# Kernel tuning notes

Hardware: AMD Instinct MI355X
Metric: run time of the kernel (lower is better)

The kernel has to match this reference:

```python
import jax, jax.numpy as jnp
import numpy as np

N_NODES, N_EDGES, HIDDEN, N_GRAPHS = 100000, 500000, 128, 2048
ATOM_DIM, BOND_DIM, OUT_DIM = 4, 3, 1


def setup_inputs() -> dict:
    key = jax.random.key(0)
    ks = jax.random.split(key, 13)
    s = 0.05  # small init scale to keep relu+scatter depth iterations numerically tame
    return {
        "x": jax.random.normal(ks[0], (N_NODES, ATOM_DIM), jnp.float32),
        "edge_index": jax.random.randint(ks[1], (2, N_EDGES), 0, N_NODES, dtype=jnp.int32),
        "edge_attr": jax.random.normal(ks[2], (N_EDGES, BOND_DIM), jnp.float32),
        "batch": jnp.sort(jax.random.randint(ks[3], (N_NODES,), 0, N_GRAPHS, dtype=jnp.int32)),
        "depth": 3,
        # DMPNN weights (bias=False)
        "W_i": jax.random.normal(ks[4], (HIDDEN, ATOM_DIM + BOND_DIM), jnp.float32) * s,
        "W_m": jax.random.normal(ks[5], (HIDDEN, HIDDEN), jnp.float32) * s,
        "W_a": jax.random.normal(ks[6], (HIDDEN, ATOM_DIM + HIDDEN), jnp.float32) * s,
        # FFN: Linear(d,4d) -> relu -> dropout(eval=identity) -> Linear(4d,d)
        "W1": jax.random.normal(ks[7], (4 * HIDDEN, HIDDEN), jnp.float32) * s,
        "b1": jnp.zeros((4 * HIDDEN,), jnp.float32),
        "W2": jax.random.normal(ks[8], (HIDDEN, 4 * HIDDEN), jnp.float32) * s,
        "b2": jnp.zeros((HIDDEN,), jnp.float32),
        "W_last": jax.random.normal(ks[9], (OUT_DIM, HIDDEN), jnp.float32) * s,
        "b_last": jnp.zeros((OUT_DIM,), jnp.float32),
    }


def reference(x, edge_index, edge_attr, batch, depth, W_i, W_m, W_a, W1, b1, W2, b2, W_last, b_last):
    src, dst = edge_index[0], edge_index[1]
    E = edge_attr.shape[0]
    N = x.shape[0]
    # h: per-edge state [E, H]
    h = jax.nn.relu(jnp.concatenate([x[src], edge_attr], axis=1) @ W_i.T)
    for _ in range(depth):
        # message: relu(W_m h) gathered at src, scatter-add to dst; PyG infers
        # dim_size from h (edge-level here), so aggregation buffer has E rows.
        m = jax.nn.relu(h @ W_m.T)
        h = h + jax.ops.segment_sum(m[src], dst, num_segments=E)
    # index_add_ edge states to nodes
    node_emb = jax.ops.segment_sum(h, dst, num_segments=N)  # [N, H]
    node_emb = jax.nn.relu(jnp.concatenate([x, node_emb], axis=1) @ W_a.T)
    # global_add_pool over graphs
    g = jax.ops.segment_sum(node_emb, batch, num_segments=N_GRAPHS)  # [G, H]
    g = jax.nn.relu(g @ W1.T + b1) @ W2.T + b2  # FFN (dropout eval = identity)
    return g @ W_last.T + b_last  # [G, OUT_DIM]
```

## Files before the change

kernel.cpp:

```cpp
#include <hip/hip_runtime.h>


#define NN 100000
#define NE 500000
#define HID 128
#define NG 2048
#define NB_SCAN 391

typedef __attribute__((ext_vector_type(8))) short bf16x8;
typedef __attribute__((ext_vector_type(4))) float f32x4;

__device__ __forceinline__ float b2f(ushort u) {
  return __uint_as_float(((uint)u) << 16);
}
__device__ __forceinline__ ushort f2b(float f) {
  uint u = __float_as_uint(f);
  return (ushort)((u + 0x7FFF + ((u >> 16) & 1)) >> 16);
}
__device__ __forceinline__ void acc8(float* a, bf16x8 v) {
#pragma unroll
  for (int j = 0; j < 8; ++j) a[j] += b2f((ushort)v[j]);
}
__device__ __forceinline__ bf16x8 pack8(const float* a) {
  bf16x8 o;
#pragma unroll
  for (int j = 0; j < 8; ++j) o[j] = (short)f2b(a[j]);
  return o;
}

__global__ __launch_bounds__(256) void k_convw(const float* __restrict__ Wm,
    const float* __restrict__ Wa, ushort* __restrict__ wmb, ushort* __restrict__ wab) {
  int i = blockIdx.x * 256 + threadIdx.x;
  if (i >= HID * HID) return;
  wmb[i] = f2b(Wm[i]);
  int c = i >> 7, k = i & 127;
  wab[i] = f2b(Wa[c * 132 + 4 + k]);
}

__global__ __launch_bounds__(256) void k_init_h(const int* __restrict__ src,
    const float* __restrict__ x, const float* __restrict__ ea,
    const float* __restrict__ Wi, ushort* __restrict__ h) {
  __shared__ float wis[HID * 7];
  for (int i = threadIdx.x; i < HID * 7; i += 256) wis[i] = Wi[i];
  __syncthreads();
  int idx = blockIdx.x * 256 + threadIdx.x;
  int e = idx >> 7, c = idx & 127;
  if (e >= NN) return;
  int s = src[e];
  const float* w = &wis[c * 7];
  float acc = x[s*4+0]*w[0] + x[s*4+1]*w[1] + x[s*4+2]*w[2] + x[s*4+3]*w[3]
            + ea[e*3+0]*w[4] + ea[e*3+1]*w[5] + ea[e*3+2]*w[6];
  h[(size_t)e * HID + c] = f2b(fmaxf(acc, 0.f));
}

__global__ __launch_bounds__(256) void k_hist2(const int* __restrict__ dst,
    int* __restrict__ cnt, int* __restrict__ cnt_lo) {
  int e = blockIdx.x * 256 + threadIdx.x;
  if (e >= NE) return;
  int d = dst[e];
  atomicAdd(&cnt[d], 1);
  if (e < NN) atomicAdd(&cnt_lo[d], 1);
}

__global__ __launch_bounds__(256) void k_scan1(const int* __restrict__ cnt,
    int* __restrict__ outp, int* __restrict__ bsums) {
  __shared__ int s[256];
  int t = threadIdx.x;
  int i = blockIdx.x * 256 + t;
  int v = (i < NN) ? cnt[i] : 0;
  s[t] = v;
  __syncthreads();
  for (int off = 1; off < 256; off <<= 1) {
    int u = (t >= off) ? s[t - off] : 0;
    __syncthreads();
    s[t] += u;
    __syncthreads();
  }
  if (i < NN) outp[i] = s[t] - v;
  if (t == 255) bsums[blockIdx.x] = s[255];
}

__global__ __launch_bounds__(512) void k_scan2(int* __restrict__ bsums) {
  __shared__ int s[512];
  int t = threadIdx.x;
  int v = (t < NB_SCAN) ? bsums[t] : 0;
  s[t] = v;
  __syncthreads();
  for (int off = 1; off < 512; off <<= 1) {
    int u = (t >= off) ? s[t - off] : 0;
    __syncthreads();
    s[t] += u;
    __syncthreads();
  }
  if (t < NB_SCAN) bsums[t] = s[t] - v;
}

__global__ __launch_bounds__(256) void k_scan3(int* __restrict__ outp,
                                               const int* __restrict__ bsums) {
  int i = blockIdx.x * 256 + threadIdx.x;
  if (i < NN) outp[i] += bsums[blockIdx.x];
  if (i == 0) outp[NN] = NE;
}

__global__ __launch_bounds__(256) void k_mid(const int* __restrict__ rowptr,
    const int* __restrict__ cnt_lo, int* __restrict__ midp) {
  int i = blockIdx.x * 256 + threadIdx.x;
  if (i < NN) midp[i] = rowptr[i] + cnt_lo[i];
}

__global__ __launch_bounds__(256) void k_fill2(const int* __restrict__ src,
    const int* __restrict__ dst, const int* __restrict__ rowptr,
    const int* __restrict__ midp, int* __restrict__ cur_lo,
    int* __restrict__ cur_hi, int* __restrict__ csr_src, int* __restrict__ csr_eid) {
  int e = blockIdx.x * 256 + threadIdx.x;
  if (e >= NE) return;
  int d = dst[e];
  int o;
  if (e < NN) o = rowptr[d] + atomicAdd(&cur_lo[d], 1);
  else        o = midp[d]   + atomicAdd(&cur_hi[d], 1);
  csr_src[o] = src[e];
  csr_eid[o] = e;
}

__global__ __launch_bounds__(256) void k_goff(const int* __restrict__ batch,
                                              int* __restrict__ goff) {
  int g = blockIdx.x * 256 + threadIdx.x;
  if (g > NG) return;
  int lo = 0, hi = NN;
  while (lo < hi) { int mid = (lo + hi) >> 1; if (batch[mid] < g) lo = mid + 1; else hi = mid; }
  goff[g] = lo;
}

template <bool HASX>
__global__ __launch_bounds__(256) void k_mfma(const ushort* __restrict__ A,
    const ushort* __restrict__ Wb, const float* __restrict__ X,
    const float* __restrict__ WaF, ushort* __restrict__ O, int nrows) {
  int tid = threadIdx.x;
  int wave = tid >> 6;
  int lane = tid & 63;
  int l15 = lane & 15, l4 = lane >> 4;
  int row0 = blockIdx.x * 64 + wave * 16;

  f32x4 acc[8];
#pragma unroll
  for (int ni = 0; ni < 8; ++ni) acc[ni] = (f32x4){0.f, 0.f, 0.f, 0.f};

  if (HASX) {
    float4 wv[8];
#pragma unroll
    for (int ni = 0; ni < 8; ++ni)
      wv[ni] = *reinterpret_cast<const float4*>(&WaF[(size_t)(ni * 16 + l15) * 132]);
#pragma unroll
    for (int j = 0; j < 4; ++j) {
      int r = row0 + l4 * 4 + j;
      if (r < nrows) {
        float4 xv = *reinterpret_cast<const float4*>(&X[(size_t)r * 4]);
#pragma unroll
        for (int ni = 0; ni < 8; ++ni)
          acc[ni][j] = xv.x * wv[ni].x + xv.y * wv[ni].y
                     + xv.z * wv[ni].z + xv.w * wv[ni].w;
      }
    }
  }

  const bf16x8 zero8 = {0, 0, 0, 0, 0, 0, 0, 0};
  int ar = row0 + l15;
#pragma unroll
  for (int k0 = 0; k0 < HID; k0 += 32) {
    bf16x8 a = (ar < nrows)
             ? *reinterpret_cast<const bf16x8*>(&A[(size_t)ar * HID + k0 + l4 * 8])
             : zero8;
    bf16x8 b[8];
#pragma unroll
    for (int ni = 0; ni < 8; ++ni)
      b[ni] = *reinterpret_cast<const bf16x8*>(&Wb[(size_t)(ni * 16 + l15) * HID + k0 + l4 * 8]);
#pragma unroll
    for (int ni = 0; ni < 8; ++ni)
      acc[ni] = __builtin_amdgcn_mfma_f32_16x16x32_bf16(a, b[ni], acc[ni], 0, 0, 0);
  }

#pragma unroll
  for (int j = 0; j < 4; ++j) {
    int r = row0 + l4 * 4 + j;
    if (r >= nrows) continue;
#pragma unroll
    for (int ni = 0; ni < 8; ++ni)
      O[(size_t)r * HID + ni * 16 + l15] = f2b(fmaxf(acc[ni][j], 0.f));
  }
}

__global__ __launch_bounds__(256) void k_gather8(const ushort* __restrict__ m,
    const int* __restrict__ rowptr, const int* __restrict__ csr_src,
    ushort* __restrict__ h) {
  int idx = blockIdx.x * 256 + threadIdx.x;
  int n = idx >> 4;
  if (n >= NN) return;
  int c8 = (idx & 15) * 8;
  float a[8];
  bf16x8 hv = *reinterpret_cast<const bf16x8*>(&h[(size_t)n * HID + c8]);
#pragma unroll
  for (int j = 0; j < 8; ++j) a[j] = b2f((ushort)hv[j]);
  int beg = rowptr[n], end = rowptr[n + 1];
  for (int i = beg; i < end; i += 8) {
    int ss[8];
#pragma unroll
    for (int k = 0; k < 8; ++k) ss[k] = csr_src[min(i + k, end - 1)];
    bf16x8 v[8];
#pragma unroll
    for (int k = 0; k < 8; ++k)
      v[k] = *reinterpret_cast<const bf16x8*>(&m[(size_t)ss[k] * HID + c8]);
#pragma unroll
    for (int k = 0; k < 8; ++k)
      if (i + k < end) acc8(a, v[k]);
  }
  *reinterpret_cast<bf16x8*>(&h[(size_t)n * HID + c8]) = pack8(a);
}

__device__ __forceinline__ void h0acc(float* a, const float w[8][7],
                                      float4 xv, float e0, float e1, float e2) {
#pragma unroll
  for (int j = 0; j < 8; ++j) {
    float t = xv.x*w[j][0] + xv.y*w[j][1] + xv.z*w[j][2] + xv.w*w[j][3]
            + e0*w[j][4] + e1*w[j][5] + e2*w[j][6];
    a[j] += fmaxf(t, 0.f);
  }
}

__global__ __launch_bounds__(256) void k_node_agg2(const ushort* __restrict__ h,
    const int* __restrict__ rowptr, const int* __restrict__ midp,
    const int* __restrict__ csr_src, const int* __restrict__ csr_eid,
    const float* __restrict__ x, const float* __restrict__ ea,
    const float* __restrict__ Wi, ushort* __restrict__ ne) {
  int idx = blockIdx.x * 256 + threadIdx.x;
  int n = idx >> 4;
  int c8 = (idx & 15) * 8;
  float w[8][7];
#pragma unroll
  for (int j = 0; j < 8; ++j)
#pragma unroll
    for (int k = 0; k < 7; ++k) w[j][k] = Wi[(c8 + j) * 7 + k];
  if (n >= NN) return;
  int beg = rowptr[n], mid = midp[n], end = rowptr[n + 1];
  float a[8];
#pragma unroll
  for (int j = 0; j < 8; ++j) a[j] = 0.f;

  for (int i = beg; i < mid; i += 4) {
    int ee[4];
#pragma unroll
    for (int k = 0; k < 4; ++k) ee[k] = csr_eid[min(i + k, mid - 1)];
    bf16x8 v[4];
#pragma unroll
    for (int k = 0; k < 4; ++k)
      v[k] = *reinterpret_cast<const bf16x8*>(&h[(size_t)ee[k] * HID + c8]);
#pragma unroll
    for (int k = 0; k < 4; ++k)
      if (i + k < mid) acc8(a, v[k]);
  }

  for (int i = mid; i < end; i += 4) {
    int s4[4], e4[4];
#pragma unroll
    for (int k = 0; k < 4; ++k) {
      int ii = min(i + k, end - 1);
      s4[k] = csr_src[ii];
      e4[k] = csr_eid[ii];
    }
    float4 xv[4];
    float ev[4][3];
#pragma unroll
    for (int k = 0; k < 4; ++k) {
      xv[k] = *reinterpret_cast<const float4*>(&x[(size_t)s4[k] * 4]);
      ev[k][0] = ea[(size_t)e4[k]*3+0];
      ev[k][1] = ea[(size_t)e4[k]*3+1];
      ev[k][2] = ea[(size_t)e4[k]*3+2];
    }
#pragma unroll
    for (int k = 0; k < 4; ++k)
      if (i + k < end) h0acc(a, w, xv[k], ev[k][0], ev[k][1], ev[k][2]);
  }
  *reinterpret_cast<bf16x8*>(&ne[(size_t)n * HID + c8]) = pack8(a);
}

__global__ __launch_bounds__(256) void k_pool(const ushort* __restrict__ na,
    const int* __restrict__ goff, float* __restrict__ g) {
  int idx = blockIdx.x * 256 + threadIdx.x;
  int gid = idx >> 4;
  if (gid >= NG) return;
  int c8 = (idx & 15) * 8;
  int beg = goff[gid], end = goff[gid + 1];
  float a[8];
#pragma unroll
  for (int j = 0; j < 8; ++j) a[j] = 0.f;
  for (int n = beg; n < end; ++n)
    acc8(a, *reinterpret_cast<const bf16x8*>(&na[(size_t)n * HID + c8]));
  *reinterpret_cast<float4*>(&g[(size_t)gid * HID + c8]) = make_float4(a[0], a[1], a[2], a[3]);
  *reinterpret_cast<float4*>(&g[(size_t)gid * HID + c8 + 4]) = make_float4(a[4], a[5], a[6], a[7]);
}

template <bool RELU>
__global__ __launch_bounds__(256) void k_gemm64(const float* __restrict__ A,
    const float* __restrict__ W, const float* __restrict__ bias,
    float* __restrict__ O, int nrows, int K, int N) {
  __shared__ float As[64][33];
  __shared__ float Bs[32][68];
  int tid = threadIdx.x;
  int row0 = blockIdx.x * 64;
  int col0 = blockIdx.y * 64;
  int tn = tid & 15;
  int tm = tid >> 4;
  float acc[4][4];
#pragma unroll
  for (int i = 0; i < 4; ++i)
#pragma unroll
    for (int j = 0; j < 4; ++j) acc[i][j] = 0.f;

  for (int k0 = 0; k0 < K; k0 += 32) {
    int ar = tid >> 3;
    int ak = (tid & 7) << 2;
#pragma unroll
    for (int rr = 0; rr < 2; ++rr) {
      int r = row0 + ar + rr * 32;
      float4 v = make_float4(0.f, 0.f, 0.f, 0.f);
      if (r < nrows) v = *reinterpret_cast<const float4*>(&A[(size_t)r * K + k0 + ak]);
      As[ar + rr*32][ak+0] = v.x; As[ar + rr*32][ak+1] = v.y;
      As[ar + rr*32][ak+2] = v.z; As[ar + rr*32][ak+3] = v.w;
    }
    int c = tid & 63;
    int kq = tid >> 6;
#pragma unroll
    for (int it = 0; it < 2; ++it) {
      int kk = kq * 4 + it * 16;
      float4 v = *reinterpret_cast<const float4*>(&W[(size_t)(col0 + c) * K + k0 + kk]);
      Bs[kk+0][c] = v.x; Bs[kk+1][c] = v.y; Bs[kk+2][c] = v.z; Bs[kk+3][c] = v.w;
    }
    __syncthreads();
#pragma unroll 8
    for (int k = 0; k < 32; ++k) {
      float av[4];
#pragma unroll
      for (int i = 0; i < 4; ++i) av[i] = As[tm*4 + i][k];
      float4 bv = *reinterpret_cast<const float4*>(&Bs[k][tn*4]);
#pragma unroll
      for (int i = 0; i < 4; ++i) {
        acc[i][0] = fmaf(av[i], bv.x, acc[i][0]);
        acc[i][1] = fmaf(av[i], bv.y, acc[i][1]);
        acc[i][2] = fmaf(av[i], bv.z, acc[i][2]);
        acc[i][3] = fmaf(av[i], bv.w, acc[i][3]);
      }
    }
    __syncthreads();
  }
#pragma unroll
  for (int i = 0; i < 4; ++i) {
    int r = row0 + tm * 4 + i;
    if (r >= nrows) continue;
    float4 o;
    int c = col0 + tn * 4;
    o.x = acc[i][0] + bias[c+0];
    o.y = acc[i][1] + bias[c+1];
    o.z = acc[i][2] + bias[c+2];
    o.w = acc[i][3] + bias[c+3];
    if (RELU) {
      o.x = fmaxf(o.x, 0.f); o.y = fmaxf(o.y, 0.f);
      o.z = fmaxf(o.z, 0.f); o.w = fmaxf(o.w, 0.f);
    }
    *reinterpret_cast<float4*>(&O[(size_t)r * N + c]) = o;
  }
}

__global__ __launch_bounds__(256) void k_last(const float* __restrict__ g3,
    const float* __restrict__ Wl, const float* __restrict__ bl,
    float* __restrict__ out) {
  int wid = (blockIdx.x * 256 + threadIdx.x) >> 6;
  int lane = threadIdx.x & 63;
  if (wid >= NG) return;
  float a = g3[(size_t)wid*128 + lane] * Wl[lane]
          + g3[(size_t)wid*128 + 64 + lane] * Wl[64 + lane];
  for (int off = 32; off; off >>= 1) a += __shfl_down(a, off);
  if (lane == 0) out[wid] = a + bl[0];
}

extern "C" void kernel_launch(void* const* d_in, const int* in_sizes, int n_in,
                              void* d_out, int out_size, void* d_ws, size_t ws_size,
                              hipStream_t stream) {
  const float* x    = (const float*)d_in[0];
  const int*   eidx = (const int*)d_in[1];
  const float* ea   = (const float*)d_in[2];
  const int*   batch= (const int*)d_in[3];
  const float* Wi   = (const float*)d_in[5];
  const float* Wm   = (const float*)d_in[6];
  const float* Wa   = (const float*)d_in[7];
  const float* W1   = (const float*)d_in[8];
  const float* b1   = (const float*)d_in[9];
  const float* W2   = (const float*)d_in[10];
  const float* b2   = (const float*)d_in[11];
  const float* Wl   = (const float*)d_in[12];
  const float* bl   = (const float*)d_in[13];
  float* out = (float*)d_out;

  const int* src = eidx;
  const int* dst = eidx + NE;

  char* p = (char*)d_ws;
  ushort* hb  = (ushort*)p; p += (size_t)NN * HID * 2;
  ushort* mb  = (ushort*)p; p += (size_t)NN * HID * 2;
  ushort* wmb = (ushort*)p; p += (size_t)HID * HID * 2;
  ushort* wab = (ushort*)p; p += (size_t)HID * HID * 2;
  float* g  = (float*)p; p += (size_t)NG * 128 * 4;
  float* g2 = (float*)p; p += (size_t)NG * 512 * 4;
  float* g3 = (float*)p; p += (size_t)NG * 128 * 4;
  int* csr_src = (int*)p; p += (size_t)NE * 4;
  int* csr_eid = (int*)p; p += (size_t)NE * 4;
  int* cnt    = (int*)p; p += (size_t)NN * 4;
  int* cnt_lo = (int*)p; p += (size_t)NN * 4;
  int* cur_lo = (int*)p; p += (size_t)NN * 4;
  int* cur_hi = (int*)p; p += (size_t)NN * 4;
  int* rowptr = (int*)p; p += (size_t)(NN + 4) * 4;
  int* midp   = (int*)p; p += (size_t)NN * 4;
  int* bsums  = (int*)p; p += 512 * 4;
  int* goff   = (int*)p; p += (size_t)(NG + 4) * 4;

  hipMemsetAsync(cnt, 0, (size_t)4 * NN * sizeof(int), stream);
  k_hist2<<<(NE + 255) / 256, 256, 0, stream>>>(dst, cnt, cnt_lo);
  k_scan1<<<NB_SCAN, 256, 0, stream>>>(cnt, rowptr, bsums);
  k_scan2<<<1, 512, 0, stream>>>(bsums);
  k_scan3<<<NB_SCAN, 256, 0, stream>>>(rowptr, bsums);
  k_mid  <<<NB_SCAN, 256, 0, stream>>>(rowptr, cnt_lo, midp);
  k_fill2<<<(NE + 255) / 256, 256, 0, stream>>>(src, dst, rowptr, midp,
                                                cur_lo, cur_hi, csr_src, csr_eid);
  k_goff <<<(NG + 256) / 256, 256, 0, stream>>>(batch, goff);

  k_convw<<<(HID * HID + 255) / 256, 256, 0, stream>>>(Wm, Wa, wmb, wab);

  k_init_h<<<(NN * HID) / 256, 256, 0, stream>>>(src, x, ea, Wi, hb);

  int ggrid = (NN + 63) / 64;
  int sgrid = (NN * 16 + 255) / 256;
  for (int it = 0; it < 3; ++it) {
    k_mfma<false><<<ggrid, 256, 0, stream>>>(hb, wmb, nullptr, nullptr, mb, NN);
    k_gather8<<<sgrid, 256, 0, stream>>>(mb, rowptr, csr_src, hb);
  }

  k_node_agg2<<<sgrid, 256, 0, stream>>>(hb, rowptr, midp, csr_src, csr_eid,
                                         x, ea, Wi, mb);
  k_mfma<true><<<ggrid, 256, 0, stream>>>(mb, wab, x, Wa, hb, NN);

  k_pool<<<(NG * 16 + 255) / 256, 256, 0, stream>>>(hb, goff, g);

  dim3 grid1((NG + 63) / 64, 512 / 64);
  k_gemm64<true><<<grid1, 256, 0, stream>>>(g, W1, b1, g2, NG, 128, 512);
  dim3 grid2((NG + 63) / 64, 128 / 64);
  k_gemm64<false><<<grid2, 256, 0, stream>>>(g2, W2, b2, g3, NG, 512, 128);
  k_last<<<(NG * 64) / 256, 256, 0, stream>>>(g3, Wl, bl, out);
}
```

Before: 485.3 us.

## Store edge/node features in 16-column planar layout for cache-local gathers

Measured after the change: 494.1 us. Within noise of the previous version (+1.8%).

```diff
diff --git a/kernel.cpp b/kernel.cpp
--- a/kernel.cpp
+++ b/kernel.cpp
@@ -6,6 +6,7 @@
 #define HID 128
 #define NG 2048
 #define NB_SCAN 391
+#define NBLKG 782
 
 typedef __attribute__((ext_vector_type(8))) short bf16x8;
 typedef __attribute__((ext_vector_type(4))) float f32x4;
@@ -26,6 +27,9 @@
 #pragma unroll
   for (int j = 0; j < 8; ++j) o[j] = (short)f2b(a[j]);
   return o;
+}
+__device__ __forceinline__ size_t taddr(int n, int c8) {
+  return ((size_t)(c8 >> 4) * NN + n) * 16 + (c8 & 8);
 }
 
 __global__ __launch_bounds__(256) void k_convw(const float* __restrict__ Wm,
@@ -39,7 +43,7 @@
 
 __global__ __launch_bounds__(256) void k_init_h(const int* __restrict__ src,
     const float* __restrict__ x, const float* __restrict__ ea,
-    const float* __restrict__ Wi, ushort* __restrict__ h) {
+    const float* __restrict__ Wi, ushort* __restrict__ hT) {
   __shared__ float wis[HID * 7];
   for (int i = threadIdx.x; i < HID * 7; i += 256) wis[i] = Wi[i];
   __syncthreads();
@@ -50,7 +54,7 @@
   const float* w = &wis[c * 7];
   float acc = x[s*4+0]*w[0] + x[s*4+1]*w[1] + x[s*4+2]*w[2] + x[s*4+3]*w[3]
             + ea[e*3+0]*w[4] + ea[e*3+1]*w[5] + ea[e*3+2]*w[6];
-  h[(size_t)e * HID + c] = f2b(fmaxf(acc, 0.f));
+  hT[((size_t)(c >> 4) * NN + e) * 16 + (c & 15)] = f2b(fmaxf(acc, 0.f));
 }
 
 __global__ __launch_bounds__(256) void k_hist2(const int* __restrict__ dst,
@@ -138,66 +142,88 @@
   int tid = threadIdx.x;
   int wave = tid >> 6;
   int lane = tid & 63;
+  int wr = wave >> 1, wc = wave & 1;
+  int row0 = blockIdx.x * 64 + wr * 32;
+  int col0 = wc * 64;
   int l15 = lane & 15, l4 = lane >> 4;
-  int row0 = blockIdx.x * 64 + wave * 16;
-
-  f32x4 acc[8];
-#pragma unroll
-  for (int ni = 0; ni < 8; ++ni) acc[ni] = (f32x4){0.f, 0.f, 0.f, 0.f};
+
+  f32x4 acc[2][4];
+#pragma unroll
+  for (int mi = 0; mi < 2; ++mi)
+#pragma unroll
+    for (int ni = 0; ni < 4; ++ni) acc[mi][ni] = (f32x4){0.f, 0.f, 0.f, 0.f};
 
   if (HASX) {
-    float4 wv[8];
-#pragma unroll
-    for (int ni = 0; ni < 8; ++ni)
-      wv[ni] = *reinterpret_cast<const float4*>(&WaF[(size_t)(ni * 16 + l15) * 132]);
+    float4 wv[4];
+#pragma unroll
+    for (int ni = 0; ni < 4; ++ni)
+      wv[ni] = *reinterpret_cast<const float4*>(&WaF[(size_t)(col0 + ni * 16 + l15) * 132]);
+#pragma unroll
+    for (int mi = 0; mi < 2; ++mi)
+#pragma unroll
+      for (int j = 0; j < 4; ++j) {
+        int r = row0 + mi * 16 + l4 * 4 + j;
+        if (r < nrows) {
+          float4 xv = *reinterpret_cast<const float4*>(&X[(size_t)r * 4]);
+#pragma unroll
+          for (int ni = 0; ni < 4; ++ni)
+            acc[mi][ni][j] = xv.x * wv[ni].x + xv.y * wv[ni].y
+                           + xv.z * wv[ni].z + xv.w * wv[ni].w;
+        }
+      }
+  }
+
+  const bf16x8 zero8 = {0, 0, 0, 0, 0, 0, 0, 0};
+#pragma unroll
+  for (int k0 = 0; k0 < HID; k0 += 32) {
+    bf16x8 a[2], b[4];
+    int c8 = k0 + l4 * 8;
+#pragma unroll
+    for (int mi = 0; mi < 2; ++mi) {
+      int r = row0 + mi * 16 + l15;
+      a[mi] = (r < nrows)
+            ? *reinterpret_cast<const bf16x8*>(&A[taddr(r, c8)])
+            : zero8;
+    }
+#pragma unroll
+    for (int ni = 0; ni < 4; ++ni) {
+      int c = col0 + ni * 16 + l15;
+      b[ni] = *reinterpret_cast<const bf16x8*>(&Wb[(size_t)c * HID + k0 + l4 * 8]);
+    }
+#pragma unroll
+    for (int mi = 0; mi < 2; ++mi)
+#pragma unroll
+      for (int ni = 0; ni < 4; ++ni)
+        acc[mi][ni] = __builtin_amdgcn_mfma_f32_16x16x32_bf16(a[mi], b[ni], acc[mi][ni], 0, 0, 0);
+  }
+
+#pragma unroll
+  for (int mi = 0; mi < 2; ++mi)
 #pragma unroll
     for (int j = 0; j < 4; ++j) {
-      int r = row0 + l4 * 4 + j;
-      if (r < nrows) {
-        float4 xv = *reinterpret_cast<const float4*>(&X[(size_t)r * 4]);
-#pragma unroll
-        for (int ni = 0; ni < 8; ++ni)
-          acc[ni][j] = xv.x * wv[ni].x + xv.y * wv[ni].y
-                     + xv.z * wv[ni].z + xv.w * wv[ni].w;
+      int r = row0 + mi * 16 + l4 * 4 + j;
+      if (r >= nrows) continue;
+#pragma unroll
+      for (int ni = 0; ni < 4; ++ni) {
+        int plane = wc * 4 + ni;
+        O[((size_t)plane * NN + r) * 16 + l15] = f2b(fmaxf(acc[mi][ni][j], 0.f));
       }
     }
-  }
-
-  const bf16x8 zero8 = {0, 0, 0, 0, 0, 0, 0, 0};
-  int ar = row0 + l15;
-#pragma unroll
-  for (int k0 = 0; k0 < HID; k0 += 32) {
-    bf16x8 a = (ar < nrows)
-             ? *reinterpret_cast<const bf16x8*>(&A[(size_t)ar * HID + k0 + l4 * 8])
-             : zero8;
-    bf16x8 b[8];
-#pragma unroll
-    for (int ni = 0; ni < 8; ++ni)
-      b[ni] = *reinterpret_cast<const bf16x8*>(&Wb[(size_t)(ni * 16 + l15) * HID + k0 + l4 * 8]);
-#pragma unroll
-    for (int ni = 0; ni < 8; ++ni)
-      acc[ni] = __builtin_amdgcn_mfma_f32_16x16x32_bf16(a, b[ni], acc[ni], 0, 0, 0);
-  }
-
-#pragma unroll
-  for (int j = 0; j < 4; ++j) {
-    int r = row0 + l4 * 4 + j;
-    if (r >= nrows) continue;
-#pragma unroll
-    for (int ni = 0; ni < 8; ++ni)
-      O[(size_t)r * HID + ni * 16 + l15] = f2b(fmaxf(acc[ni][j], 0.f));
-  }
-}
-
-__global__ __launch_bounds__(256) void k_gather8(const ushort* __restrict__ m,
+}
+
+__global__ __launch_bounds__(256) void k_gather_t(const ushort* __restrict__ mT,
     const int* __restrict__ rowptr, const int* __restrict__ csr_src,
-    ushort* __restrict__ h) {
-  int idx = blockIdx.x * 256 + threadIdx.x;
-  int n = idx >> 4;
+    ushort* __restrict__ hT) {
+  int t = blockIdx.x / NBLKG;
+  int b = blockIdx.x % NBLKG;
+  int p = threadIdx.x >> 1;
+  int half8 = (threadIdx.x & 1) * 8;
+  int n = b * 128 + p;
   if (n >= NN) return;
-  int c8 = (idx & 15) * 8;
+  size_t plane = (size_t)t * NN;
+  size_t base = (plane + n) * 16 + half8;
   float a[8];
-  bf16x8 hv = *reinterpret_cast<const bf16x8*>(&h[(size_t)n * HID + c8]);
+  bf16x8 hv = *reinterpret_cast<const bf16x8*>(&hT[base]);
 #pragma unroll
   for (int j = 0; j < 8; ++j) a[j] = b2f((ushort)hv[j]);
   int beg = rowptr[n], end = rowptr[n + 1];
@@ -208,12 +234,12 @@
     bf16x8 v[8];
 #pragma unroll
     for (int k = 0; k < 8; ++k)
-      v[k] = *reinterpret_cast<const bf16x8*>(&m[(size_t)ss[k] * HID + c8]);
+      v[k] = *reinterpret_cast<const bf16x8*>(&mT[(plane + ss[k]) * 16 + half8]);
 #pragma unroll
     for (int k = 0; k < 8; ++k)
       if (i + k < end) acc8(a, v[k]);
   }
-  *reinterpret_cast<bf16x8*>(&h[(size_t)n * HID + c8]) = pack8(a);
+  *reinterpret_cast<bf16x8*>(&hT[base]) = pack8(a);
 }
 
 __device__ __forceinline__ void h0acc(float* a, const float w[8][7],
@@ -252,7 +278,7 @@
     bf16x8 v[4];
 #pragma unroll
     for (int k = 0; k < 4; ++k)
-      v[k] = *reinterpret_cast<const bf16x8*>(&h[(size_t)ee[k] * HID + c8]);
+      v[k] = *reinterpret_cast<const bf16x8*>(&h[taddr(ee[k], c8)]);
 #pragma unroll
     for (int k = 0; k < 4; ++k)
       if (i + k < mid) acc8(a, v[k]);
@@ -279,7 +305,7 @@
     for (int k = 0; k < 4; ++k)
       if (i + k < end) h0acc(a, w, xv[k], ev[k][0], ev[k][1], ev[k][2]);
   }
-  *reinterpret_cast<bf16x8*>(&ne[(size_t)n * HID + c8]) = pack8(a);
+  *reinterpret_cast<bf16x8*>(&ne[taddr(n, c8)]) = pack8(a);
 }
 
 __global__ __launch_bounds__(256) void k_pool(const ushort* __restrict__ na,
@@ -288,12 +314,14 @@
   int gid = idx >> 4;
   if (gid >= NG) return;
   int c8 = (idx & 15) * 8;
+  size_t pbase = (size_t)(c8 >> 4) * NN;
+  int off = c8 & 8;
   int beg = goff[gid], end = goff[gid + 1];
   float a[8];
 #pragma unroll
   for (int j = 0; j < 8; ++j) a[j] = 0.f;
   for (int n = beg; n < end; ++n)
-    acc8(a, *reinterpret_cast<const bf16x8*>(&na[(size_t)n * HID + c8]));
+    acc8(a, *reinterpret_cast<const bf16x8*>(&na[(pbase + n) * 16 + off]));
   *reinterpret_cast<float4*>(&g[(size_t)gid * HID + c8]) = make_float4(a[0], a[1], a[2], a[3]);
   *reinterpret_cast<float4*>(&g[(size_t)gid * HID + c8 + 4]) = make_float4(a[4], a[5], a[6], a[7]);
 }
@@ -436,14 +464,13 @@
   k_init_h<<<(NN * HID) / 256, 256, 0, stream>>>(src, x, ea, Wi, hb);
 
   int ggrid = (NN + 63) / 64;
-  int sgrid = (NN * 16 + 255) / 256;
   for (int it = 0; it < 3; ++it) {
     k_mfma<false><<<ggrid, 256, 0, stream>>>(hb, wmb, nullptr, nullptr, mb, NN);
-    k_gather8<<<sgrid, 256, 0, stream>>>(mb, rowptr, csr_src, hb);
-  }
-
-  k_node_agg2<<<sgrid, 256, 0, stream>>>(hb, rowptr, midp, csr_src, csr_eid,
-                                         x, ea, Wi, mb);
+    k_gather_t<<<8 * NBLKG, 256, 0, stream>>>(mb, rowptr, csr_src, hb);
+  }
+
+  k_node_agg2<<<(NN * 16 + 255) / 256, 256, 0, stream>>>(hb, rowptr, midp,
+                                                csr_src, csr_eid, x, ea, Wi, mb);
   k_mfma<true><<<ggrid, 256, 0, stream>>>(mb, wab, x, Wa, hb, NN);
 
   k_pool<<<(NG * 16 + 255) / 256, 256, 0, stream>>>(hb, goff, g);
```
